# Optimization experiments

Hardware: AMD Instinct MI355X
Metric: run time of the kernel (lower is better)

The kernel has to match this reference:

```python
import jax, jax.numpy as jnp
import numpy as np
import math

B, T, E, H = 64, 256, 1024, 16
HD = E // H  # 64
EPS = 1e-5


def layernorm(x, g, b):
    mu = jnp.mean(x, axis=-1, keepdims=True)
    var = jnp.mean(jnp.square(x - mu), axis=-1, keepdims=True)
    return (x - mu) * jax.lax.rsqrt(var + EPS) * g + b


def setup_inputs() -> dict:
    key = jax.random.key(0)
    ks = jax.random.split(key, 10)
    s = 0.02
    return {
        "x": jax.random.normal(ks[0], (B, T, E), dtype=jnp.float32),
        "ln1_g": jnp.ones((E,), jnp.float32),
        "ln1_b": jnp.zeros((E,), jnp.float32),
        "wk": jax.random.normal(ks[1], (H, E, HD), jnp.float32) * s,
        "wq": jax.random.normal(ks[2], (H, E, HD), jnp.float32) * s,
        "wv": jax.random.normal(ks[3], (H, E, HD), jnp.float32) * s,
        "w_proj": jax.random.normal(ks[4], (E, E), jnp.float32) * s,
        "b_proj": jnp.zeros((E,), jnp.float32),
        "ln2_g": jnp.ones((E,), jnp.float32),
        "ln2_b": jnp.zeros((E,), jnp.float32),
        "w1": jax.random.normal(ks[5], (E, E), jnp.float32) * s,
        "b1": jnp.zeros((E,), jnp.float32),
        "w2": jax.random.normal(ks[6], (E, E), jnp.float32) * s,
        "b2": jnp.zeros((E,), jnp.float32),
    }


def reference(x, ln1_g, ln1_b, wk, wq, wv, w_proj, b_proj, ln2_g, ln2_b, w1, b1, w2, b2):
    # --- multi-head causal attention on LN1(x) ---
    h = layernorm(x, ln1_g, ln1_b)
    k = jnp.einsum('bte,hed->bhtd', h, wk)
    q = jnp.einsum('bte,hed->bhtd', h, wq)
    v = jnp.einsum('bte,hed->bhtd', h, wv)
    # NOTE: original computes k @ q^T (K.Q^T), not the standard Q.K^T -- kept faithful
    scores = jnp.einsum('bhtd,bhsd->bhts', k, q) / math.sqrt(HD)
    mask = jnp.tril(jnp.ones((T, T), dtype=bool))
    scores = jnp.where(mask, scores, -jnp.inf)
    attn_w = jax.nn.softmax(scores, axis=-1)  # dropout = identity in eval
    attn = jnp.einsum('bhts,bhsd->bhtd', attn_w, v)
    attn = attn.transpose(0, 2, 1, 3).reshape(B, T, E)  # concat heads
    x = x + attn @ w_proj + b_proj
    # --- feed-forward on LN2(x) ---
    h2 = layernorm(x, ln2_g, ln2_b)
    ff = jax.nn.relu(h2 @ w1 + b1) @ w2 + b2
    return x + ff
```

## Files before the change

kernel.cpp:

```cpp
#include <hip/hip_runtime.h>

typedef unsigned int u32;
typedef unsigned short u16;
typedef __attribute__((ext_vector_type(8))) short bf16x8;
typedef __attribute__((ext_vector_type(4))) float f32x4;

#define GLOBAL_AS __attribute__((address_space(1)))
#define LDS_AS    __attribute__((address_space(3)))

#define B_   64
#define T_   256
#define E_   1024
#define H_   16
#define HD_  64
#define NTOK (B_*T_)
#define K_   1024
#define LNEPS 1e-5f

__device__ __forceinline__ u16 f2bf(float f){
  u32 x = __float_as_uint(f);
  u32 r = x + 0x7fffu + ((x >> 16) & 1u);
  return (u16)(r >> 16);
}
__device__ __forceinline__ u16 f2bf_trunc(float f){
  return (u16)(__float_as_uint(f) >> 16);
}
__device__ __forceinline__ u32 pack2(float a, float b){
  return (u32)f2bf(a) | ((u32)f2bf(b) << 16);
}

__device__ __forceinline__ void gload16(const u16* g, u16* l){
  __builtin_amdgcn_global_load_lds((const GLOBAL_AS void*)g, (LDS_AS void*)l, 16, 0, 0);
}

__global__ __launch_bounds__(256) void ln_bf16_kernel(
    const float* __restrict__ x, const float* __restrict__ g,
    const float* __restrict__ b, u16* __restrict__ o)
{
  int lane  = threadIdx.x & 63;
  int token = (blockIdx.x << 2) + (threadIdx.x >> 6);
  const float4* xr = (const float4*)(x + (size_t)token * E_);
  float4 v[4];
  float s = 0.f, ss = 0.f;
  #pragma unroll
  for (int i = 0; i < 4; ++i){
    v[i] = xr[lane + 64 * i];
    s += v[i].x + v[i].y + v[i].z + v[i].w;
    ss = fmaf(v[i].x, v[i].x, fmaf(v[i].y, v[i].y,
         fmaf(v[i].z, v[i].z, fmaf(v[i].w, v[i].w, ss))));
  }
  #pragma unroll
  for (int off = 32; off > 0; off >>= 1){
    s  += __shfl_xor(s,  off);
    ss += __shfl_xor(ss, off);
  }
  float mu   = s * (1.f / E_);
  float var  = ss * (1.f / E_) - mu * mu;
  float rstd = rsqrtf(var + LNEPS);
  const float4* gr = (const float4*)g;
  const float4* br = (const float4*)b;
  uint2* orow = (uint2*)(o + (size_t)token * E_);
  #pragma unroll
  for (int i = 0; i < 4; ++i){
    float4 gg = gr[lane + 64 * i], bb = br[lane + 64 * i];
    float y0 = (v[i].x - mu) * rstd * gg.x + bb.x;
    float y1 = (v[i].y - mu) * rstd * gg.y + bb.y;
    float y2 = (v[i].z - mu) * rstd * gg.z + bb.z;
    float y3 = (v[i].w - mu) * rstd * gg.w + bb.w;
    orow[lane + 64 * i] = make_uint2(pack2(y0, y1), pack2(y2, y3));
  }
}

__global__ __launch_bounds__(256) void convq_kernel(
    const float* __restrict__ wk, const float* __restrict__ wq,
    const float* __restrict__ wv, u16* __restrict__ o)
{
  __shared__ float tile[64 * 68];
  const int zh = blockIdx.x, z = zh >> 4, h = zh & 15;
  const int k0 = blockIdx.y << 6;
  const float* w = (z == 0 ? wk : z == 1 ? wq : wv) + (size_t)h * (E_ * HD_);
  const int t = threadIdx.x;
  {
    int kr = t >> 2, d0 = (t & 3) << 4;
    const float4* src = (const float4*)(w + (size_t)(k0 + kr) * HD_ + d0);
    #pragma unroll
    for (int i = 0; i < 4; ++i)
      *(float4*)(tile + kr * 68 + d0 + 4 * i) = src[i];
  }
  __syncthreads();
  {
    const size_t nb32 = (size_t)zh * 32 + (k0 >> 5);
    #pragma unroll
    for (int u = 0; u < 2; ++u) {
      int cid = t * 2 + u;
      int dd = cid >> 3, kc = cid & 7;
      u32 wd[4];
      #pragma unroll
      for (int e2 = 0; e2 < 4; ++e2)
        wd[e2] = pack2(tile[(kc * 8 + 2 * e2) * 68 + dd],
                       tile[(kc * 8 + 2 * e2 + 1) * 68 + dd]);
      u16* dst = o + (nb32 + (kc >> 2)) * 2048 + (size_t)(dd >> 4) * 512
                   + (size_t)(((kc & 3) << 4) + (dd & 15)) * 8;
      *(uint4*)dst = make_uint4(wd[0], wd[1], wd[2], wd[3]);
    }
  }
}

__global__ __launch_bounds__(256) void convt_kernel(
    const float* __restrict__ w, u16* __restrict__ o)
{
  __shared__ float tile[64 * 68];
  const int n0 = blockIdx.x << 6, k0 = blockIdx.y << 6;
  const int t = threadIdx.x;
  {
    int kr = t >> 2, nn = (t & 3) << 4;
    const float4* src = (const float4*)(w + (size_t)(k0 + kr) * E_ + n0 + nn);
    #pragma unroll
    for (int i = 0; i < 4; ++i)
      *(float4*)(tile + kr * 68 + nn + 4 * i) = src[i];
  }
  __syncthreads();
  {
    const size_t nb32 = (size_t)(n0 >> 6) * 32 + (k0 >> 5);
    #pragma unroll
    for (int u = 0; u < 2; ++u) {
      int cid = t * 2 + u;
      int dd = cid >> 3, kc = cid & 7;
      u32 wd[4];
      #pragma unroll
      for (int e2 = 0; e2 < 4; ++e2)
        wd[e2] = pack2(tile[(kc * 8 + 2 * e2) * 68 + dd],
                       tile[(kc * 8 + 2 * e2 + 1) * 68 + dd]);
      u16* dst = o + (nb32 + (kc >> 2)) * 2048 + (size_t)(dd >> 4) * 512
                   + (size_t)(((kc & 3) << 4) + (dd & 15)) * 8;
      *(uint4*)dst = make_uint4(wd[0], wd[1], wd[2], wd[3]);
    }
  }
}

#define MF4(I, AV, BV)                                                               \
  acc[I][0] = __builtin_amdgcn_mfma_f32_16x16x32_bf16(AV, BV[0], acc[I][0], 0, 0, 0);\
  acc[I][1] = __builtin_amdgcn_mfma_f32_16x16x32_bf16(AV, BV[1], acc[I][1], 0, 0, 0);\
  acc[I][2] = __builtin_amdgcn_mfma_f32_16x16x32_bf16(AV, BV[2], acc[I][2], 0, 0, 0);\
  acc[I][3] = __builtin_amdgcn_mfma_f32_16x16x32_bf16(AV, BV[3], acc[I][3], 0, 0, 0);

#define BLOADS(BV, SS) {                                                      \
    const u16* bp_ = Bp + (size_t)(SS) * 2048;                                \
    BV[0] = *(const bf16x8*)(bp_);                                            \
    BV[1] = *(const bf16x8*)(bp_ + 512);                                      \
    BV[2] = *(const bf16x8*)(bp_ + 1024);                                     \
    BV[3] = *(const bf16x8*)(bp_ + 1536);                                     \
  }

#define MSLICE2(SLOT, NSLOT, KA, DO_STAGE, DO_NXT, DO_BL, BS, ACUR, ATMP, ANXT, BV, BNV, VM) { \
    const u16* As_ = lds + (SLOT) * 8192;                                     \
          \
    ATMP[0] = *(const bf16x8*)(As_ + aoffb + 2048);                           \
    ATMP[1] = *(const bf16x8*)(As_ + aoffb + 2560);                           \
    ATMP[2] = *(const bf16x8*)(As_ + aoffb + 3072);                           \
    ATMP[3] = *(const bf16x8*)(As_ + aoffb + 3584);                           \
    if (DO_STAGE) {                                                           \
      u16* d_ = lds + (((SLOT) + 3) & 3) * 8192;                              \
      gload16(Ag0 + (KA), d_ + tid * 8);                                      \
      gload16(Ag1 + (KA), d_ + 4096 + tid * 8);                               \
    }                                                                         \
    __builtin_amdgcn_s_setprio(1);                                            \
    MF4(0, ACUR[0], BV) MF4(1, ACUR[1], BV) MF4(2, ACUR[2], BV) MF4(3, ACUR[3], BV) \
    __builtin_amdgcn_s_setprio(0);                                            \
             \
    if (DO_NXT) {                                                             \
      const u16* An_ = lds + (NSLOT) * 8192;                                  \
      ANXT[0] = *(const bf16x8*)(An_ + aoffb);                                \
      ANXT[1] = *(const bf16x8*)(An_ + aoffb + 512);                          \
      ANXT[2] = *(const bf16x8*)(An_ + aoffb + 1024);                         \
      ANXT[3] = *(const bf16x8*)(An_ + aoffb + 1536);                         \
    }                                                                         \
    __builtin_amdgcn_s_setprio(1);                                            \
    MF4(4, ATMP[0], BV) MF4(5, ATMP[1], BV) MF4(6, ATMP[2], BV) MF4(7, ATMP[3], BV) \
    __builtin_amdgcn_s_setprio(0);                                            \
    if (DO_BL) { BLOADS(BNV, BS) }                                            \
    VM;                                                                       \
    __builtin_amdgcn_s_barrier();                                             \
    __builtin_amdgcn_sched_barrier(0);                                        \
    asm volatile("" ::: "memory");                                            \
  }

#define VM10 asm volatile("s_waitcnt vmcnt(10)" ::: "memory")
#define VM8  asm volatile("s_waitcnt vmcnt(8)"  ::: "memory")
#define VM4  asm volatile("s_waitcnt vmcnt(4)"  ::: "memory")

template<int MODE>
__global__ __launch_bounds__(512, 2) void mgemm_kernel(
    const u16* __restrict__ A, const u16* __restrict__ Bt,
    const float* __restrict__ bias, const float* __restrict__ resid,
    float* __restrict__ Cf, u16* __restrict__ Cb, u16* __restrict__ Cb2)
{
  __shared__ __align__(16) u16 lds[65536];

  const int tid = threadIdx.x, lane = tid & 63, wid = tid >> 6;
  const int wm = wid >> 2, wn = wid & 3;
  const int l15 = lane & 15, quad = lane >> 4;

  const int b = (int)blockIdx.x;
  const int xcd = b & 7, ib = b >> 3;
  const int row0 = ((xcd << 3) + (ib & 7)) << 8;
  const int col0 = (ib >> 3) << 8;

  const int sc   = (tid & 7) ^ ((tid >> 3) & 7);
  const int srow = 2 * (tid >> 3) + (sc >> 2);
  const int skof = (sc & 3) << 3;
  const u16* Ag0 = A + (size_t)(row0 + srow) * K_ + skof;
  const u16* Ag1 = Ag0 + (size_t)128 * K_;

  const int rhalf = l15 >> 1;
  const int cph   = ((((l15 & 1) << 2) | quad) ^ rhalf);
  const int aoffb = wm * 4096 + rhalf * 64 + cph * 8;

  const u16* Bp = Bt + (size_t)((col0 >> 6) + wn) * 65536 + lane * 8;

  f32x4 acc[8][4];
  #pragma unroll
  for (int i = 0; i < 8; ++i)
    #pragma unroll
    for (int j = 0; j < 4; ++j)
      acc[i][j] = (f32x4){0.f, 0.f, 0.f, 0.f};

  bf16x8 aA[4], aB[4], aT[4], bE[4], bO[4];

  #pragma unroll
  for (int t3 = 0; t3 < 3; ++t3) {
    u16* d_ = lds + t3 * 8192;
    gload16(Ag0 + t3 * 32, d_ + tid * 8);
    gload16(Ag1 + t3 * 32, d_ + 4096 + tid * 8);
  }
  BLOADS(bE, 0)
  BLOADS(bO, 1)
  asm volatile("s_waitcnt vmcnt(10)" ::: "memory");
  __builtin_amdgcn_s_barrier();
  __builtin_amdgcn_sched_barrier(0);
  asm volatile("" ::: "memory");

  aA[0] = *(const bf16x8*)(lds + aoffb);
  aA[1] = *(const bf16x8*)(lds + aoffb + 512);
  aA[2] = *(const bf16x8*)(lds + aoffb + 1024);
  aA[3] = *(const bf16x8*)(lds + aoffb + 1536);

  #pragma unroll 1
  for (int s = 0; s < 28; s += 2) {
    MSLICE2(s & 3, (s + 1) & 3, (s + 3) * 32, 1, 1, 1, s + 2, aA, aT, aB, bE, bE, VM10)
    MSLICE2((s + 1) & 3, (s + 2) & 3, (s + 4) * 32, 1, 1, 1, s + 3, aB, aT, aA, bO, bO, VM10)
  }
  MSLICE2(0, 1, 31 * 32, 1, 1, 1, 30, aA, aT, aB, bE, bE, VM10)
  MSLICE2(1, 2, 0,       0, 1, 1, 31, aB, aT, aA, bO, bO, VM8 )
  MSLICE2(2, 3, 0,       0, 1, 0, 0,  aA, aT, aB, bE, bE, VM4 )
  MSLICE2(3, 0, 0,       0, 0, 0, 0,  aB, aT, aA, bO, bO, (void)0)

  if (MODE == 1 || MODE == 3) {
    const int rbase = row0 + wm * 128;
    #pragma unroll
    for (int j = 0; j < 4; ++j) {
      const int n = col0 + wn * 64 + j * 16 + l15;
      const float bn = bias[n];
      #pragma unroll
      for (int i = 0; i < 8; ++i)
        #pragma unroll
        for (int r = 0; r < 4; ++r) {
          const int row = rbase + i * 16 + quad * 4 + r;
          const size_t idx = (size_t)row * E_ + n;
          float v = acc[i][j][r] + bn;
          if (MODE == 1) Cf[idx] = v + resid[idx];
          else           Cf[idx] = v + Cf[idx];
        }
    }
    return;
  }

  u16* ep = lds + wid * 8192;
  const int nb0 = col0 + wn * 64;

  if (MODE == 2) {
    #pragma unroll
    for (int j = 0; j < 4; ++j) {
      const float bn = bias[nb0 + j * 16 + l15];
      #pragma unroll
      for (int i = 0; i < 8; ++i)
        #pragma unroll
        for (int r = 0; r < 4; ++r)
          ep[(i*16 + quad*4 + r) * 64 + j*16 + l15] =
              f2bf(fmaxf(acc[i][j][r] + bn, 0.f));
    }
    __syncthreads();
    const int rbase = row0 + wm * 128;
    #pragma unroll
    for (int it = 0; it < 16; ++it) {
      const int tl = it * 8 + (lane >> 3), c = lane & 7;
      uint4 v = *(const uint4*)(ep + tl * 64 + c * 8);
      *(uint4*)(Cb + (size_t)(rbase + tl) * E_ + nb0 + c * 8) = v;
    }
    return;
  }

  const int z = nb0 >> 10, hh = (nb0 >> 6) & 15;
  const int rows0 = row0 + wm * 128;
  const int bb = rows0 >> 8, tb0 = rows0 & 255;
  if (z < 2) {
    #pragma unroll
    for (int i = 0; i < 8; ++i)
      #pragma unroll
      for (int j = 0; j < 4; ++j)
        #pragma unroll
        for (int r = 0; r < 4; ++r)
          ep[(i*16 + quad*4 + r) * 64 + j*16 + l15] = f2bf(acc[i][j][r]);
    __syncthreads();
    u16* out = (z == 0 ? Cb : Cb2) + ((size_t)(bb * H_ + hh) * T_ + tb0) * HD_;
    #pragma unroll
    for (int it = 0; it < 16; ++it) {
      const int tl = it * 8 + (lane >> 3), c = lane & 7;
      uint4 v = *(const uint4*)(ep + tl * 64 + c * 8);
      *(uint4*)(out + (size_t)tl * HD_ + c * 8) = v;
    }
  } else {
    #pragma unroll
    for (int i = 0; i < 8; ++i)
      #pragma unroll
      for (int j = 0; j < 4; ++j)
        #pragma unroll
        for (int r = 0; r < 4; ++r) {
          const int tl = i*16 + quad*4 + r, d = j*16 + l15;
          const int phys = (tl >> 3) ^ (d & 15);
          ep[d * 128 + phys * 8 + (tl & 7)] = f2bf(acc[i][j][r]);
        }
    __syncthreads();
    u16* out = (u16*)Cf + ((size_t)(bb * H_ + hh) * HD_) * T_;
    #pragma unroll
    for (int it = 0; it < 16; ++it) {
      const int d = it * 4 + (lane >> 4), c = lane & 15;
      const int phys = c ^ (d & 15);
      uint4 v = *(const uint4*)(ep + d * 128 + phys * 8);
      *(uint4*)(out + (size_t)d * T_ + tb0 + c * 8) = v;
    }
  }
}

__global__ __launch_bounds__(256) void fattn_kernel(
    const u16* __restrict__ kk_, const u16* __restrict__ qq_,
    const u16* __restrict__ vt_, u16* __restrict__ out)
{
  __shared__ __align__(16) u16 Pb[4][64 * 72];
  const int tid = threadIdx.x, lane = tid & 63, wv = tid >> 6;
  const int bh = blockIdx.x * 4 + wv;
  const int tblk = blockIdx.y;
  const int l15 = lane & 15, quad = lane >> 4;
  const u16* kb  = kk_ + (size_t)bh * (T_ * HD_);
  const u16* qb  = qq_ + (size_t)bh * (T_ * HD_);
  const u16* vtb = vt_ + (size_t)bh * (HD_ * T_);
  u16* Pw = Pb[wv];

  bf16x8 kf[4][2];
  #pragma unroll
  for (int i = 0; i < 4; ++i)
    #pragma unroll
    for (int c = 0; c < 2; ++c)
      kf[i][c] = *(const bf16x8*)(kb + (size_t)(tblk*64 + i*16 + l15) * HD_ + c*32 + quad*8);

  f32x4 o[4][4];
  float mrow[4][4], lrow[4][4];
  #pragma unroll
  for (int i = 0; i < 4; ++i) {
    #pragma unroll
    for (int j = 0; j < 4; ++j) o[i][j] = (f32x4){0.f, 0.f, 0.f, 0.f};
    #pragma unroll
    for (int r = 0; r < 4; ++r) { mrow[i][r] = -1e30f; lrow[i][r] = 0.f; }
  }

  for (int sb = 0; sb <= tblk; ++sb) {
    f32x4 S[4][4];
    #pragma unroll
    for (int j = 0; j < 4; ++j) {
      bf16x8 qf0 = *(const bf16x8*)(qb + (size_t)(sb*64 + j*16 + l15) * HD_ +      quad*8);
      bf16x8 qf1 = *(const bf16x8*)(qb + (size_t)(sb*64 + j*16 + l15) * HD_ + 32 + quad*8);
      #pragma unroll
      for (int i = 0; i < 4; ++i) {
        f32x4 t0 = __builtin_amdgcn_mfma_f32_16x16x32_bf16(kf[i][0], qf0,
                       (f32x4){0.f,0.f,0.f,0.f}, 0, 0, 0);
        S[i][j] = __builtin_amdgcn_mfma_f32_16x16x32_bf16(kf[i][1], qf1, t0, 0, 0, 0);
      }
    }
    #pragma unroll
    for (int i = 0; i < 4; ++i)
      #pragma unroll
      for (int j = 0; j < 4; ++j)
        #pragma unroll
        for (int r = 0; r < 4; ++r) {
          float val = S[i][j][r] * 0.125f;
          if (sb == tblk) {
            int tl = i*16 + quad*4 + r, sl = j*16 + l15;
            if (sl > tl) val = -1e30f;
          }
          S[i][j][r] = val;
        }
    #pragma unroll
    for (int i = 0; i < 4; ++i)
      #pragma unroll
      for (int r = 0; r < 4; ++r) {
        float mx = fmaxf(fmaxf(S[i][0][r], S[i][1][r]), fmaxf(S[i][2][r], S[i][3][r]));
        #pragma unroll
        for (int msk = 1; msk < 16; msk <<= 1) mx = fmaxf(mx, __shfl_xor(mx, msk));
        float mn = fmaxf(mrow[i][r], mx);
        float al = __expf(mrow[i][r] - mn);
        mrow[i][r] = mn;
        float sm = 0.f;
        #pragma unroll
        for (int j = 0; j < 4; ++j) {
          float p = __expf(S[i][j][r] - mn);
          S[i][j][r] = p;
          sm += p;
        }
        #pragma unroll
        for (int msk = 1; msk < 16; msk <<= 1) sm += __shfl_xor(sm, msk);
        lrow[i][r] = lrow[i][r] * al + sm;
        #pragma unroll
        for (int jd = 0; jd < 4; ++jd) o[i][jd][r] *= al;
      }
    #pragma unroll
    for (int i = 0; i < 4; ++i)
      #pragma unroll
      for (int j = 0; j < 4; ++j)
        #pragma unroll
        for (int r = 0; r < 4; ++r)
          Pw[(i*16 + quad*4 + r) * 72 + j*16 + l15] = f2bf_trunc(S[i][j][r]);
    bf16x8 pf[4][2];
    #pragma unroll
    for (int i = 0; i < 4; ++i)
      #pragma unroll
      for (int c = 0; c < 2; ++c)
        pf[i][c] = *(const bf16x8*)(Pw + (i*16 + l15) * 72 + c*32 + quad*8);
    #pragma unroll
    for (int jd = 0; jd < 4; ++jd) {
      bf16x8 vf0 = *(const bf16x8*)(vtb + (size_t)(jd*16 + l15) * T_ + sb*64 +      quad*8);
      bf16x8 vf1 = *(const bf16x8*)(vtb + (size_t)(jd*16 + l15) * T_ + sb*64 + 32 + quad*8);
      #pragma unroll
      for (int i = 0; i < 4; ++i) {
        f32x4 t0 = __builtin_amdgcn_mfma_f32_16x16x32_bf16(pf[i][0], vf0, o[i][jd], 0, 0, 0);
        o[i][jd] = __builtin_amdgcn_mfma_f32_16x16x32_bf16(pf[i][1], vf1, t0, 0, 0, 0);
      }
    }
  }

  #pragma unroll
  for (int i = 0; i < 4; ++i)
    #pragma unroll
    for (int r = 0; r < 4; ++r) {
      float inv = 1.0f / lrow[i][r];
      #pragma unroll
      for (int jd = 0; jd < 4; ++jd)
        Pw[(i*16 + quad*4 + r) * 72 + jd*16 + l15] = f2bf(o[i][jd][r] * inv);
    }
  {
    const int b = bh >> 4, h = bh & 15;
    const uint4* pr = (const uint4*)(Pw + lane * 72);
    uint4* og = (uint4*)(out + ((size_t)(b * T_ + tblk*64 + lane)) * E_ + h * HD_);
    #pragma unroll
    for (int k = 0; k < 8; ++k) og[k] = pr[k];
  }
}

extern "C" void kernel_launch(void* const* d_in, const int* in_sizes, int n_in,
                              void* d_out, int out_size, void* d_ws, size_t ws_size,
                              hipStream_t stream) {
  const float* x     = (const float*)d_in[0];
  const float* ln1g  = (const float*)d_in[1];
  const float* ln1b  = (const float*)d_in[2];
  const float* wk    = (const float*)d_in[3];
  const float* wq    = (const float*)d_in[4];
  const float* wv    = (const float*)d_in[5];
  const float* wproj = (const float*)d_in[6];
  const float* bproj = (const float*)d_in[7];
  const float* ln2g  = (const float*)d_in[8];
  const float* ln2b  = (const float*)d_in[9];
  const float* w1    = (const float*)d_in[10];
  const float* b1    = (const float*)d_in[11];
  const float* w2    = (const float*)d_in[12];
  const float* b2    = (const float*)d_in[13];
  float* outp = (float*)d_out;

  char* ws = (char*)d_ws;
  const size_t MB = 1024 * 1024;
  u16* wqkvT  = (u16*)(ws);
  u16* wprojT = (u16*)(ws + 6 * MB);
  u16* w1T    = (u16*)(ws + 8 * MB);
  u16* w2T    = (u16*)(ws + 10 * MB);
  u16* hb     = (u16*)(ws + 16 * MB);
  u16* kbuf   = (u16*)(ws + 48 * MB);
  u16* qbuf   = (u16*)(ws + 80 * MB);
  u16* vtbuf  = (u16*)d_out;

  convq_kernel<<<dim3(48, 16), 256, 0, stream>>>(wk, wq, wv, wqkvT);
  convt_kernel<<<dim3(16, 16), 256, 0, stream>>>(wproj, wprojT);
  convt_kernel<<<dim3(16, 16), 256, 0, stream>>>(w1, w1T);
  convt_kernel<<<dim3(16, 16), 256, 0, stream>>>(w2, w2T);

  ln_bf16_kernel<<<NTOK/4, 256, 0, stream>>>(x, ln1g, ln1b, hb);
  mgemm_kernel<0><<<768, 512, 0, stream>>>(
      hb, wqkvT, nullptr, nullptr, (float*)vtbuf, kbuf, qbuf);
  fattn_kernel<<<dim3(B_*H_/4, 4), 256, 0, stream>>>(kbuf, qbuf, vtbuf, hb);
  mgemm_kernel<1><<<256, 512, 0, stream>>>(
      hb, wprojT, bproj, x, outp, nullptr, nullptr);
  ln_bf16_kernel<<<NTOK/4, 256, 0, stream>>>(outp, ln2g, ln2b, kbuf);
  mgemm_kernel<2><<<256, 512, 0, stream>>>(
      kbuf, w1T, b1, nullptr, nullptr, qbuf, nullptr);
  mgemm_kernel<3><<<256, 512, 0, stream>>>(
      qbuf, w2T, b2, nullptr, outp, nullptr, nullptr);
}
```

Measured before the change: 513.1 us.

## Shrink GEMM tiles to 128x128 with 256-thread blocks for more blocks and occupancy

Changes the bf16 MFMA GEMM from 256x256 tiles with 8 waves to 128x128 tiles with 4 waves. LDS staging, accumulators, the block-to-tile mapping and the epilogues are resized to match, and grids grow fourfold. The aim is more blocks per CU and better load balance across the chip. In exchange, arithmetic intensity per tile drops, so more global and L2 traffic is needed for the same work. The removed __syncthreads in the epilogues rely on each wave owning its own LDS region, but that region now overlaps A-staging slots other waves may still be reading.

```diff
diff --git a/kernel.cpp b/kernel.cpp
--- a/kernel.cpp
+++ b/kernel.cpp
@@ -153,30 +153,26 @@
   }
 
 #define MSLICE2(SLOT, NSLOT, KA, DO_STAGE, DO_NXT, DO_BL, BS, ACUR, ATMP, ANXT, BV, BNV, VM) { \
-    const u16* As_ = lds + (SLOT) * 8192;                                     \
+    const u16* As_ = lds + (SLOT) * 4096;                                     \
           \
-    ATMP[0] = *(const bf16x8*)(As_ + aoffb + 2048);                           \
-    ATMP[1] = *(const bf16x8*)(As_ + aoffb + 2560);                           \
-    ATMP[2] = *(const bf16x8*)(As_ + aoffb + 3072);                           \
-    ATMP[3] = *(const bf16x8*)(As_ + aoffb + 3584);                           \
+    ATMP[0] = *(const bf16x8*)(As_ + aoffb + 1024);                           \
+    ATMP[1] = *(const bf16x8*)(As_ + aoffb + 1536);                           \
     if (DO_STAGE) {                                                           \
-      u16* d_ = lds + (((SLOT) + 3) & 3) * 8192;                              \
+      u16* d_ = lds + (((SLOT) + 3) & 3) * 4096;                              \
       gload16(Ag0 + (KA), d_ + tid * 8);                                      \
-      gload16(Ag1 + (KA), d_ + 4096 + tid * 8);                               \
+      gload16(Ag1 + (KA), d_ + 2048 + tid * 8);                               \
     }                                                                         \
     __builtin_amdgcn_s_setprio(1);                                            \
-    MF4(0, ACUR[0], BV) MF4(1, ACUR[1], BV) MF4(2, ACUR[2], BV) MF4(3, ACUR[3], BV) \
+    MF4(0, ACUR[0], BV) MF4(1, ACUR[1], BV)                                   \
     __builtin_amdgcn_s_setprio(0);                                            \
              \
     if (DO_NXT) {                                                             \
-      const u16* An_ = lds + (NSLOT) * 8192;                                  \
+      const u16* An_ = lds + (NSLOT) * 4096;                                  \
       ANXT[0] = *(const bf16x8*)(An_ + aoffb);                                \
       ANXT[1] = *(const bf16x8*)(An_ + aoffb + 512);                          \
-      ANXT[2] = *(const bf16x8*)(An_ + aoffb + 1024);                         \
-      ANXT[3] = *(const bf16x8*)(An_ + aoffb + 1536);                         \
     }                                                                         \
     __builtin_amdgcn_s_setprio(1);                                            \
-    MF4(4, ATMP[0], BV) MF4(5, ATMP[1], BV) MF4(6, ATMP[2], BV) MF4(7, ATMP[3], BV) \
+    MF4(2, ATMP[0], BV) MF4(3, ATMP[1], BV)                                   \
     __builtin_amdgcn_s_setprio(0);                                            \
     if (DO_BL) { BLOADS(BNV, BS) }                                            \
     VM;                                                                       \
@@ -190,48 +186,50 @@
 #define VM4  asm volatile("s_waitcnt vmcnt(4)"  ::: "memory")
 
 template<int MODE>
-__global__ __launch_bounds__(512, 2) void mgemm_kernel(
+__global__ __launch_bounds__(256, 3) void mgemm_kernel(
     const u16* __restrict__ A, const u16* __restrict__ Bt,
     const float* __restrict__ bias, const float* __restrict__ resid,
     float* __restrict__ Cf, u16* __restrict__ Cb, u16* __restrict__ Cb2)
 {
-  __shared__ __align__(16) u16 lds[65536];
+  __shared__ __align__(16) u16 lds[16384];
 
   const int tid = threadIdx.x, lane = tid & 63, wid = tid >> 6;
-  const int wm = wid >> 2, wn = wid & 3;
+  const int wm = wid >> 1, wn = wid & 1;
   const int l15 = lane & 15, quad = lane >> 4;
 
+  const int NT = (MODE == 0) ? 24 : 8;
   const int b = (int)blockIdx.x;
   const int xcd = b & 7, ib = b >> 3;
-  const int row0 = ((xcd << 3) + (ib & 7)) << 8;
-  const int col0 = (ib >> 3) << 8;
+  const int mloc = ib / NT, ntile = ib - mloc * NT;
+  const int row0 = (xcd * 16 + mloc) << 7;
+  const int col0 = ntile << 7;
 
   const int sc   = (tid & 7) ^ ((tid >> 3) & 7);
   const int srow = 2 * (tid >> 3) + (sc >> 2);
   const int skof = (sc & 3) << 3;
   const u16* Ag0 = A + (size_t)(row0 + srow) * K_ + skof;
-  const u16* Ag1 = Ag0 + (size_t)128 * K_;
+  const u16* Ag1 = Ag0 + (size_t)64 * K_;
 
   const int rhalf = l15 >> 1;
   const int cph   = ((((l15 & 1) << 2) | quad) ^ rhalf);
-  const int aoffb = wm * 4096 + rhalf * 64 + cph * 8;
+  const int aoffb = wm * 2048 + rhalf * 64 + cph * 8;
 
   const u16* Bp = Bt + (size_t)((col0 >> 6) + wn) * 65536 + lane * 8;
 
-  f32x4 acc[8][4];
-  #pragma unroll
-  for (int i = 0; i < 8; ++i)
+  f32x4 acc[4][4];
+  #pragma unroll
+  for (int i = 0; i < 4; ++i)
     #pragma unroll
     for (int j = 0; j < 4; ++j)
       acc[i][j] = (f32x4){0.f, 0.f, 0.f, 0.f};
 
-  bf16x8 aA[4], aB[4], aT[4], bE[4], bO[4];
+  bf16x8 aA[2], aB[2], aT[2], bE[4], bO[4];
 
   #pragma unroll
   for (int t3 = 0; t3 < 3; ++t3) {
-    u16* d_ = lds + t3 * 8192;
+    u16* d_ = lds + t3 * 4096;
     gload16(Ag0 + t3 * 32, d_ + tid * 8);
-    gload16(Ag1 + t3 * 32, d_ + 4096 + tid * 8);
+    gload16(Ag1 + t3 * 32, d_ + 2048 + tid * 8);
   }
   BLOADS(bE, 0)
   BLOADS(bO, 1)
@@ -242,8 +240,6 @@
 
   aA[0] = *(const bf16x8*)(lds + aoffb);
   aA[1] = *(const bf16x8*)(lds + aoffb + 512);
-  aA[2] = *(const bf16x8*)(lds + aoffb + 1024);
-  aA[3] = *(const bf16x8*)(lds + aoffb + 1536);
 
   #pragma unroll 1
   for (int s = 0; s < 28; s += 2) {
@@ -256,13 +252,13 @@
   MSLICE2(3, 0, 0,       0, 0, 0, 0,  aB, aT, aA, bO, bO, (void)0)
 
   if (MODE == 1 || MODE == 3) {
-    const int rbase = row0 + wm * 128;
+    const int rbase = row0 + wm * 64;
     #pragma unroll
     for (int j = 0; j < 4; ++j) {
       const int n = col0 + wn * 64 + j * 16 + l15;
       const float bn = bias[n];
       #pragma unroll
-      for (int i = 0; i < 8; ++i)
+      for (int i = 0; i < 4; ++i)
         #pragma unroll
         for (int r = 0; r < 4; ++r) {
           const int row = rbase + i * 16 + quad * 4 + r;
@@ -275,7 +271,7 @@
     return;
   }
 
-  u16* ep = lds + wid * 8192;
+  u16* ep = lds + wid * 4096;
   const int nb0 = col0 + wn * 64;
 
   if (MODE == 2) {
@@ -283,16 +279,15 @@
     for (int j = 0; j < 4; ++j) {
       const float bn = bias[nb0 + j * 16 + l15];
       #pragma unroll
-      for (int i = 0; i < 8; ++i)
+      for (int i = 0; i < 4; ++i)
         #pragma unroll
         for (int r = 0; r < 4; ++r)
           ep[(i*16 + quad*4 + r) * 64 + j*16 + l15] =
               f2bf(fmaxf(acc[i][j][r] + bn, 0.f));
     }
-    __syncthreads();
-    const int rbase = row0 + wm * 128;
-    #pragma unroll
-    for (int it = 0; it < 16; ++it) {
+    const int rbase = row0 + wm * 64;
+    #pragma unroll
+    for (int it = 0; it < 8; ++it) {
       const int tl = it * 8 + (lane >> 3), c = lane & 7;
       uint4 v = *(const uint4*)(ep + tl * 64 + c * 8);
       *(uint4*)(Cb + (size_t)(rbase + tl) * E_ + nb0 + c * 8) = v;
@@ -301,43 +296,41 @@
   }
 
   const int z = nb0 >> 10, hh = (nb0 >> 6) & 15;
-  const int rows0 = row0 + wm * 128;
-  const int bb = rows0 >> 8, tb0 = rows0 & 255;
+  const int rows0 = row0 + wm * 64;
+  const int bb = rows0 >> 8, tb = rows0 & 255;
   if (z < 2) {
     #pragma unroll
-    for (int i = 0; i < 8; ++i)
+    for (int i = 0; i < 4; ++i)
       #pragma unroll
       for (int j = 0; j < 4; ++j)
         #pragma unroll
         for (int r = 0; r < 4; ++r)
           ep[(i*16 + quad*4 + r) * 64 + j*16 + l15] = f2bf(acc[i][j][r]);
-    __syncthreads();
-    u16* out = (z == 0 ? Cb : Cb2) + ((size_t)(bb * H_ + hh) * T_ + tb0) * HD_;
-    #pragma unroll
-    for (int it = 0; it < 16; ++it) {
+    u16* out = (z == 0 ? Cb : Cb2) + ((size_t)(bb * H_ + hh) * T_ + tb) * HD_;
+    #pragma unroll
+    for (int it = 0; it < 8; ++it) {
       const int tl = it * 8 + (lane >> 3), c = lane & 7;
       uint4 v = *(const uint4*)(ep + tl * 64 + c * 8);
       *(uint4*)(out + (size_t)tl * HD_ + c * 8) = v;
     }
   } else {
     #pragma unroll
-    for (int i = 0; i < 8; ++i)
+    for (int i = 0; i < 4; ++i)
       #pragma unroll
       for (int j = 0; j < 4; ++j)
         #pragma unroll
         for (int r = 0; r < 4; ++r) {
           const int tl = i*16 + quad*4 + r, d = j*16 + l15;
-          const int phys = (tl >> 3) ^ (d & 15);
-          ep[d * 128 + phys * 8 + (tl & 7)] = f2bf(acc[i][j][r]);
+          const int cs = (tl >> 3) ^ (d & 7);
+          ep[d * 64 + cs * 8 + (tl & 7)] = f2bf(acc[i][j][r]);
         }
-    __syncthreads();
     u16* out = (u16*)Cf + ((size_t)(bb * H_ + hh) * HD_) * T_;
     #pragma unroll
-    for (int it = 0; it < 16; ++it) {
-      const int d = it * 4 + (lane >> 4), c = lane & 15;
-      const int phys = c ^ (d & 15);
-      uint4 v = *(const uint4*)(ep + d * 128 + phys * 8);
-      *(uint4*)(out + (size_t)d * T_ + tb0 + c * 8) = v;
+    for (int it = 0; it < 8; ++it) {
+      const int d = it * 8 + (lane >> 3), c = lane & 7;
+      const int cs = c ^ (d & 7);
+      uint4 v = *(const uint4*)(ep + d * 64 + cs * 8);
+      *(uint4*)(out + (size_t)d * T_ + tb + c * 8) = v;
     }
   }
 }
@@ -501,14 +494,14 @@
   convt_kernel<<<dim3(16, 16), 256, 0, stream>>>(w2, w2T);
 
   ln_bf16_kernel<<<NTOK/4, 256, 0, stream>>>(x, ln1g, ln1b, hb);
-  mgemm_kernel<0><<<768, 512, 0, stream>>>(
+  mgemm_kernel<0><<<3072, 256, 0, stream>>>(
       hb, wqkvT, nullptr, nullptr, (float*)vtbuf, kbuf, qbuf);
   fattn_kernel<<<dim3(B_*H_/4, 4), 256, 0, stream>>>(kbuf, qbuf, vtbuf, hb);
-  mgemm_kernel<1><<<256, 512, 0, stream>>>(
+  mgemm_kernel<1><<<1024, 256, 0, stream>>>(
       hb, wprojT, bproj, x, outp, nullptr, nullptr);
   ln_bf16_kernel<<<NTOK/4, 256, 0, stream>>>(outp, ln2g, ln2b, kbuf);
-  mgemm_kernel<2><<<256, 512, 0, stream>>>(
+  mgemm_kernel<2><<<1024, 256, 0, stream>>>(
       kbuf, w1T, b1, nullptr, nullptr, qbuf, nullptr);
-  mgemm_kernel<3><<<256, 512, 0, stream>>>(
+  mgemm_kernel<3><<<1024, 256, 0, stream>>>(
       qbuf, w2T, b2, nullptr, outp, nullptr, nullptr);
 }
```

Result: no change. 520.5 us (+1.5%).
